# Kernel tuning notes

Hardware: AMD Instinct MI355X
Metric: run time of the kernel (lower is better)

Reference implementation:

```python
import jax, jax.numpy as jnp
import numpy as np

EMBED_DIM = 512
NUM_HEADS = 8
WINDOW = 128
B, S = 4, 2048


def setup_inputs() -> dict:
    key = jax.random.key(0)
    k0, k1, k2, k3, k4 = jax.random.split(key, 5)
    scale = 1.0 / np.sqrt(EMBED_DIM)
    return {
        "embeddings": jax.random.normal(k0, (B, S, EMBED_DIM), dtype=jnp.float32),
        "in_proj_w": jax.random.normal(k1, (3 * EMBED_DIM, EMBED_DIM), dtype=jnp.float32) * scale,
        "in_proj_b": jax.random.normal(k2, (3 * EMBED_DIM,), dtype=jnp.float32) * 0.01,
        "out_w": jax.random.normal(k3, (EMBED_DIM, EMBED_DIM), dtype=jnp.float32) * scale,
        "out_b": jax.random.normal(k4, (EMBED_DIM,), dtype=jnp.float32) * 0.01,
    }


def reference(embeddings, in_proj_w, in_proj_b, out_w, out_b):
    b, s, e = embeddings.shape
    h = NUM_HEADS
    dh = e // h
    # combined QKV projection (matches torch nn.MultiheadAttention in_proj)
    qkv = embeddings @ in_proj_w.T + in_proj_b          # [b,s,3e]
    q, k, v = jnp.split(qkv, 3, axis=-1)
    q = q.reshape(b, s, h, dh)
    k = k.reshape(b, s, h, dh)
    v = v.reshape(b, s, h, dh)
    scores = jnp.einsum("bihd,bjhd->bhij", q, k) / jnp.sqrt(jnp.float32(dh))
    # banded window mask: position i attends to [i-W, i+W]
    idx = jnp.arange(s)
    band = jnp.abs(idx[:, None] - idx[None, :]) <= WINDOW   # [s,s] bool
    scores = jnp.where(band, scores, -jnp.inf)
    attn = jax.nn.softmax(scores, axis=-1)                   # [b,h,s,s]
    ctx = jnp.einsum("bhij,bjhd->bihd", attn, v).reshape(b, s, e)
    out = ctx @ out_w.T + out_b                              # [b,s,e]
    pooled = jnp.max(out, axis=1)                            # [b,e]
    weights = jnp.mean(attn, axis=1)                         # head-averaged [b,s,s]
    return pooled, weights
```

## Files before the change

kernel.cpp:

```cpp
#include <hip/hip_runtime.h>
#include <math.h>

#define BB   4
#define SS   2048
#define EE   512
#define HH   8
#define DH   64
#define WW   128
#define MM   (BB*SS)
#define NTILE (SS/32)
#define SWH  296
#define VTP  296
#define WST  49
#define BK   64

typedef _Float16 f16x8 __attribute__((ext_vector_type(8)));
typedef _Float16 f16x2 __attribute__((ext_vector_type(2)));
typedef float    f32x4 __attribute__((ext_vector_type(4)));

#define GLOAD16(gp, lp) __builtin_amdgcn_global_load_lds( \
    (const __attribute__((address_space(1))) void*)(gp),  \
    (__attribute__((address_space(3))) void*)(lp), 16, 0, 0)

__global__ __launch_bounds__(256) void convert3(
    const float* __restrict__ a, const float* __restrict__ bsrc,
    const float* __restrict__ c,
    _Float16* __restrict__ da, _Float16* __restrict__ db, _Float16* __restrict__ dc)
{
    const size_t na4 = (size_t)MM*EE/4;
    const size_t nb4 = (size_t)3*EE*EE/4;
    const size_t nc4 = (size_t)EE*EE/4;
    const size_t tot = na4 + nb4 + nc4;
    for (size_t i = (size_t)blockIdx.x*256 + threadIdx.x; i < tot;
         i += (size_t)gridDim.x*256) {
        const float* s; _Float16* d; size_t off;
        if (i < na4)            { s = a;    d = da; off = i; }
        else if (i < na4 + nb4) { s = bsrc; d = db; off = i - na4; }
        else                    { s = c;    d = dc; off = i - na4 - nb4; }
        float4 v = ((const float4*)s)[off];
        union { _Float16 h[4]; uint2 u; } o;
        o.h[0] = (_Float16)v.x; o.h[1] = (_Float16)v.y;
        o.h[2] = (_Float16)v.z; o.h[3] = (_Float16)v.w;
        ((uint2*)d)[off] = o.u;
    }
}

__global__ __launch_bounds__(256) void qkv_mfma(
    const _Float16* __restrict__ A, const _Float16* __restrict__ Wt,
    const float* __restrict__ bias,
    _Float16* __restrict__ qd, _Float16* __restrict__ kd, _Float16* __restrict__ vd)
{
    __shared__ _Float16 As[128*BK];
    __shared__ _Float16 Bs[128*BK];

    const int tid = threadIdx.x;
    const int wid = tid >> 6, lane = tid & 63;
    const int l15 = lane & 15, g = lane >> 4;
    const int wr = wid >> 1, wc = wid & 1;
    const int m0 = blockIdx.x * 128;
    const int n0 = blockIdx.y * 128;

    const int lrow = lane >> 3;
    const int swz  = (lane & 7) ^ lrow;
    const _Float16* Ab = A  + (size_t)(m0 + wid*32 + lrow)*512 + swz*8;
    const _Float16* Bb = Wt + (size_t)(n0 + wid*32 + lrow)*512 + swz*8;

    f32x4 acc[4][4] = {};
    for (int k0 = 0; k0 < 512; k0 += BK) {
        __syncthreads();
        #pragma unroll
        for (int t = 0; t < 4; ++t) {
            GLOAD16(Ab + (size_t)t*8*512 + k0, &As[(wid*32 + t*8)*BK]);
            GLOAD16(Bb + (size_t)t*8*512 + k0, &Bs[(wid*32 + t*8)*BK]);
        }
        __syncthreads();

        f16x8 af[2][4], bf[2][4];
        #pragma unroll
        for (int ks = 0; ks < 2; ++ks)
            #pragma unroll
            for (int f = 0; f < 4; ++f) {
                const int ch = ((ks*4 + g) ^ (l15 & 7)) * 8;
                af[ks][f] = *(const f16x8*)&As[(wr*64 + f*16 + l15)*BK + ch];
                bf[ks][f] = *(const f16x8*)&Bs[(wc*64 + f*16 + l15)*BK + ch];
            }
        #pragma unroll
        for (int ks = 0; ks < 2; ++ks)
            #pragma unroll
            for (int fi = 0; fi < 4; ++fi)
                #pragma unroll
                for (int fj = 0; fj < 4; ++fj)
                    acc[fi][fj] = __builtin_amdgcn_mfma_f32_16x16x32_f16(
                        af[ks][fi], bf[ks][fj], acc[fi][fj], 0, 0, 0);
    }

    const int which = n0 >> 9;
    _Float16* dst = (which == 0) ? qd : (which == 1) ? kd : vd;
    #pragma unroll
    for (int fj = 0; fj < 4; ++fj) {
        const int col = n0 + wc*64 + fj*16 + l15;
        const int h = (col >> 6) & 7;
        const float bc = bias[col];
        #pragma unroll
        for (int fi = 0; fi < 4; ++fi)
            #pragma unroll
            for (int rr = 0; rr < 4; ++rr) {
                int grow = m0 + wr*64 + fi*16 + g*4 + rr;
                int b = grow >> 11, s = grow & 2047;
                dst[(((size_t)(b*HH + h))*SS + s)*DH + (col & 63)] =
                    (_Float16)(acc[fi][fj][rr] + bc);
            }
    }
}

__global__ __launch_bounds__(256) void out_mfma(
    const _Float16* __restrict__ A, const _Float16* __restrict__ Wt,
    const float* __restrict__ bias, float* __restrict__ part)
{
    __shared__ _Float16 As[128*BK];
    __shared__ _Float16 Bs[128*BK];

    const int tid = threadIdx.x;
    const int wid = tid >> 6, lane = tid & 63;
    const int l15 = lane & 15, g = lane >> 4;
    const int wr = wid >> 1, wc = wid & 1;
    const int m0 = blockIdx.x * 128;
    const int n0 = blockIdx.y * 128;

    const int lrow = lane >> 3;
    const int swz  = (lane & 7) ^ lrow;
    const _Float16* Ab = A  + (size_t)(m0 + wid*32 + lrow)*512 + swz*8;
    const _Float16* Bb = Wt + (size_t)(n0 + wid*32 + lrow)*512 + swz*8;

    f32x4 acc[4][4] = {};
    for (int k0 = 0; k0 < 512; k0 += BK) {
        __syncthreads();
        #pragma unroll
        for (int t = 0; t < 4; ++t) {
            GLOAD16(Ab + (size_t)t*8*512 + k0, &As[(wid*32 + t*8)*BK]);
            GLOAD16(Bb + (size_t)t*8*512 + k0, &Bs[(wid*32 + t*8)*BK]);
        }
        __syncthreads();

        f16x8 af[2][4], bf[2][4];
        #pragma unroll
        for (int ks = 0; ks < 2; ++ks)
            #pragma unroll
            for (int f = 0; f < 4; ++f) {
                const int ch = ((ks*4 + g) ^ (l15 & 7)) * 8;
                af[ks][f] = *(const f16x8*)&As[(wr*64 + f*16 + l15)*BK + ch];
                bf[ks][f] = *(const f16x8*)&Bs[(wc*64 + f*16 + l15)*BK + ch];
            }
        #pragma unroll
        for (int ks = 0; ks < 2; ++ks)
            #pragma unroll
            for (int fi = 0; fi < 4; ++fi)
                #pragma unroll
                for (int fj = 0; fj < 4; ++fj)
                    acc[fi][fj] = __builtin_amdgcn_mfma_f32_16x16x32_f16(
                        af[ks][fi], bf[ks][fj], acc[fi][fj], 0, 0, 0);
    }

    __syncthreads();
    float* red = (float*)As;
    #pragma unroll
    for (int fj = 0; fj < 4; ++fj) {
        float cm = -1e30f;
        #pragma unroll
        for (int fi = 0; fi < 4; ++fi)
            #pragma unroll
            for (int rr = 0; rr < 4; ++rr)
                cm = fmaxf(cm, acc[fi][fj][rr]);
        cm = fmaxf(cm, __shfl_xor(cm, 16));
        cm = fmaxf(cm, __shfl_xor(cm, 32));
        if (g == 0) red[wr*128 + wc*64 + fj*16 + l15] = cm;
    }
    __syncthreads();
    if (tid < 128) {
        float m = fmaxf(red[tid], red[128 + tid]) + bias[n0 + tid];
        part[(size_t)blockIdx.x * EE + n0 + tid] = m;
    }
}

__global__ __launch_bounds__(512, 4) void attn_mfma(
    const _Float16* __restrict__ qd, const _Float16* __restrict__ kd,
    const _Float16* __restrict__ vd, _Float16* __restrict__ ctx,
    float2* __restrict__ stats)
{
    __shared__ _Float16 sc[32 * SWH];
    __shared__ _Float16 vt[64 * VTP];

    const int tid  = threadIdx.x;
    const int wid  = tid >> 6;
    const int lane = tid & 63;
    const int l15  = lane & 15;
    const int g    = lane >> 4;

    const int lin = blockIdx.x + (blockIdx.y << 6) + (blockIdx.z << 8);
    const int nid = (lin & 7) * 256 + (lin >> 3);
    const int ti = nid & 63;
    const int b  = (nid >> 6) & 3;
    const int h  = nid >> 8;

    const int i0 = ti * 32;
    const int jlo = (i0 - WW > 0) ? i0 - WW : 0;
    const int jhi = (i0 + 31 + WW < SS - 1) ? i0 + 31 + WW : SS - 1;
    const int nj = jhi - jlo + 1;
    const int NC = nj >> 4;

    const _Float16* qb = qd + ((size_t)(b*HH + h))*SS*DH;
    const _Float16* kb = kd + ((size_t)(b*HH + h))*SS*DH;
    const _Float16* vb = vd + ((size_t)(b*HH + h))*SS*DH;

    for (int idx = tid; idx < 288*8; idx += 512) {
        int row = idx >> 3, dg = idx & 7;
        int d0 = dg * 8;
        int j = jlo + row;
        f16x8 vv = {};
        if (j <= jhi) vv = *(const f16x8*)(vb + (size_t)j*DH + d0);
        int blk = row >> 3, off = row & 7;
        int xb = (blk < 32) ? (blk ^ dg) : blk;
        _Float16* col = &vt[(size_t)d0*VTP + xb*8 + off];
        #pragma unroll
        for (int e = 0; e < 8; ++e)
            col[e*VTP] = vv[e];
    }

    if (nj < 288) {
        int row = tid >> 4, pt = tid & 15;
        for (int jj = nj + pt; jj < 288; jj += 16)
            sc[row*SWH + jj] = (_Float16)(-60000.f);
    }

    {
        const int rh = wid & 1, cgrp = wid >> 1;
        const int qrow = i0 + rh*16 + l15;
        f16x8 aq0 = *(const f16x8*)(qb + (size_t)qrow*DH +      g*8);
        f16x8 aq1 = *(const f16x8*)(qb + (size_t)qrow*DH + 32 + g*8);
        #pragma unroll
        for (int t = 0; t < 5; ++t) {
            int c = cgrp + t*4;
            if (c < NC) {
                int jj = c*16 + l15;
                int j  = jlo + jj;
                f16x8 bk0 = *(const f16x8*)(kb + (size_t)j*DH +      g*8);
                f16x8 bk1 = *(const f16x8*)(kb + (size_t)j*DH + 32 + g*8);
                f32x4 s = {0.f, 0.f, 0.f, 0.f};
                s = __builtin_amdgcn_mfma_f32_16x16x32_f16(aq0, bk0, s, 0, 0, 0);
                s = __builtin_amdgcn_mfma_f32_16x16x32_f16(aq1, bk1, s, 0, 0, 0);
                #pragma unroll
                for (int r = 0; r < 4; ++r) {
                    int srow = rh*16 + g*4 + r;
                    int i = i0 + srow;
                    int dd = i - j; if (dd < 0) dd = -dd;
                    float val = (dd <= WW) ? s[r]*0.125f : -60000.f;
                    sc[srow*SWH + jj] = (_Float16)val;
                }
            }
        }
    }
    __syncthreads();

    {
        const int qi = tid >> 4, pt = tid & 15;
        _Float16* srow = &sc[qi*SWH];
        f16x8 v0 = *(const f16x8*)&srow[pt*16];
        f16x8 v1 = *(const f16x8*)&srow[pt*16 + 8];
        f16x2 v2 = *(const f16x2*)&srow[256 + pt*2];
        float x[18];
        #pragma unroll
        for (int e = 0; e < 8; ++e) { x[e] = (float)v0[e]; x[8+e] = (float)v1[e]; }
        x[16] = (float)v2[0]; x[17] = (float)v2[1];

        float mrow = x[0];
        #pragma unroll
        for (int e = 1; e < 18; ++e) mrow = fmaxf(mrow, x[e]);
        #pragma unroll
        for (int o = 1; o < 16; o <<= 1) mrow = fmaxf(mrow, __shfl_xor(mrow, o));

        float ssum = 0.f;
        #pragma unroll
        for (int e = 0; e < 18; ++e) { x[e] = __expf(x[e] - mrow); ssum += x[e]; }
        #pragma unroll
        for (int o = 1; o < 16; o <<= 1) ssum += __shfl_xor(ssum, o);
        const float inv = 1.0f / ssum;

        f16x8 p0, p1;
        f16x2 p2;
        #pragma unroll
        for (int e = 0; e < 8; ++e) {
            p0[e] = (_Float16)(x[e]   * inv);
            p1[e] = (_Float16)(x[8+e] * inv);
        }
        p2[0] = (_Float16)(x[16] * inv);
        p2[1] = (_Float16)(x[17] * inv);
        *(f16x8*)&srow[pt*16]      = p0;
        *(f16x8*)&srow[pt*16 + 8]  = p1;
        *(f16x2*)&srow[256 + pt*2] = p2;
        if (pt == 0)
            stats[((size_t)(b*HH + h))*SS + i0 + qi] = make_float2(mrow, inv);
    }
    __syncthreads();

    {
        const int rh = wid & 1, dt = wid >> 1;
        const int d = dt*16 + l15;
        const int dg = d >> 3;
        f32x4 acc = {0.f, 0.f, 0.f, 0.f};
        #pragma unroll
        for (int ks = 0; ks < 9; ++ks) {
            int blk = ks*4 + g;
            int xb = (blk < 32) ? (blk ^ dg) : blk;
            f16x8 ap = *(const f16x8*)&sc[(rh*16 + l15)*SWH + ks*32 + g*8];
            f16x8 bv = *(const f16x8*)&vt[(size_t)d*VTP + xb*8];
            acc = __builtin_amdgcn_mfma_f32_16x16x32_f16(ap, bv, acc, 0, 0, 0);
        }
        #pragma unroll
        for (int r = 0; r < 4; ++r) {
            int row = i0 + rh*16 + g*4 + r;
            ctx[((size_t)(b*SS + row))*EE + h*DH + dt*16 + l15] = (_Float16)acc[r];
        }
    }
}

__global__ __launch_bounds__(256) void weights_k(
    const _Float16* __restrict__ qd, const _Float16* __restrict__ kd,
    const float2* __restrict__ stats, float* __restrict__ wout)
{
    __shared__ float wacc[32 * WST];

    const int tid  = threadIdx.x;
    const int wid  = tid >> 6;
    const int lane = tid & 63;
    const int l15  = lane & 15;
    const int g    = lane >> 4;

    const int lin = blockIdx.x + (blockIdx.y << 6) + (blockIdx.z << 8);
    const int nid = (lin & 7) * 192 + (lin >> 3);
    const int ti = nid & 63;
    const int b  = (nid >> 6) & 3;
    const int z  = nid >> 8;

    const int i0 = ti * 32;
    const int jlo = (i0 - WW > 0) ? i0 - WW : 0;
    const int jhi = (i0 + 31 + WW < SS - 1) ? i0 + 31 + WW : SS - 1;
    const int nj = jhi - jlo + 1;
    const int NC = nj >> 4;

    {
        const int L = jlo;
        const int Z = SS - nj;
        const int zrow = tid >> 3;
        const int zpt  = tid & 7;
        float* wrow = wout + ((size_t)(b*SS + i0 + zrow))*SS;
        int vend = (z + 1) * 320; if (vend > Z) vend = Z;
        const float4 zf = make_float4(0.f, 0.f, 0.f, 0.f);
        for (int v4 = z*320 + zpt*4; v4 < vend; v4 += 32) {
            int col = (v4 < L) ? v4 : (jhi + 1 + (v4 - L));
            *(float4*)(wrow + col) = zf;
        }
    }

    const int rh = wid & 1, cg2 = wid >> 1;
    const int qrow = i0 + rh*16 + l15;

    float ws[2][4];
    #pragma unroll
    for (int t = 0; t < 2; ++t)
        #pragma unroll
        for (int r = 0; r < 4; ++r) ws[t][r] = 0.f;

    for (int h = 0; h < HH; ++h) {
        const _Float16* qb = qd + ((size_t)(b*HH + h))*SS*DH;
        const _Float16* kb = kd + ((size_t)(b*HH + h))*SS*DH;
        f16x8 aq0 = *(const f16x8*)(qb + (size_t)qrow*DH +      g*8);
        f16x8 aq1 = *(const f16x8*)(qb + (size_t)qrow*DH + 32 + g*8);
        float2 st[4];
        #pragma unroll
        for (int r = 0; r < 4; ++r)
            st[r] = stats[((size_t)(b*HH + h))*SS + i0 + rh*16 + g*4 + r];

        #pragma unroll
        for (int t = 0; t < 2; ++t) {
            int lt = cg2 + t*2;
            int c = z*3 + lt;
            if (lt < 3 && c < NC) {
                int jj = c*16 + l15;
                int j  = jlo + jj;
                f16x8 bk0 = *(const f16x8*)(kb + (size_t)j*DH +      g*8);
                f16x8 bk1 = *(const f16x8*)(kb + (size_t)j*DH + 32 + g*8);
                f32x4 s = {0.f, 0.f, 0.f, 0.f};
                s = __builtin_amdgcn_mfma_f32_16x16x32_f16(aq0, bk0, s, 0, 0, 0);
                s = __builtin_amdgcn_mfma_f32_16x16x32_f16(aq1, bk1, s, 0, 0, 0);
                #pragma unroll
                for (int r = 0; r < 4; ++r) {
                    int i = i0 + rh*16 + g*4 + r;
                    int dd = i - j; if (dd < 0) dd = -dd;
                    if (dd <= WW)
                        ws[t][r] += __expf(s[r]*0.125f - st[r].x) * st[r].y;
                }
            }
        }
    }

    #pragma unroll
    for (int t = 0; t < 2; ++t) {
        int lt = cg2 + t*2, c = z*3 + lt;
        if (lt < 3 && c < NC) {
            #pragma unroll
            for (int r = 0; r < 4; ++r)
                wacc[(rh*16 + g*4 + r)*WST + lt*16 + l15] = ws[t][r];
        }
    }
    __syncthreads();

    const int cbase = jlo + z*48;
    int lo = cbase, hi = cbase + 48;
    if (hi > SS) hi = SS;

    const int row = tid >> 3;
    const int pt  = tid & 7;
    const int i = i0 + row;
    const int blo = (i - WW > 0) ? i - WW : 0;
    const int bhi = (i + WW < SS - 1) ? i + WW : SS - 1;
    float* wrow = wout + ((size_t)(b*SS + i))*SS;
    for (int j4 = lo + pt*4; j4 < hi; j4 += 32) {
        float4 o;
        float* oo = (float*)&o;
        #pragma unroll
        for (int e = 0; e < 4; ++e) {
            int j = j4 + e;
            oo[e] = (j >= blo && j <= bhi)
                  ? wacc[row*WST + (j - cbase)] * 0.125f : 0.f;
        }
        *(float4*)(wrow + j4) = o;
    }
}

__global__ void pool_final(const float* __restrict__ part, float* __restrict__ pooled)
{
    int e = blockIdx.x * 256 + threadIdx.x;
    int b = blockIdx.y;
    float m = -1e30f;
    #pragma unroll
    for (int t = 0; t < 16; ++t)
        m = fmaxf(m, part[((size_t)(b*16 + t))*EE + e]);
    pooled[b*EE + e] = m;
}

extern "C" void kernel_launch(void* const* d_in, const int* in_sizes, int n_in,
                              void* d_out, int out_size, void* d_ws, size_t ws_size,
                              hipStream_t stream)
{
    const float* emb = (const float*)d_in[0];
    const float* ipw = (const float*)d_in[1];
    const float* ipb = (const float*)d_in[2];
    const float* ow  = (const float*)d_in[3];
    const float* ob  = (const float*)d_in[4];

    float* pooled = (float*)d_out;
    float* wout   = pooled + (size_t)BB*EE;

    const size_t headsz = (size_t)BB*HH*SS*DH;
    _Float16* q    = (_Float16*)d_ws;
    _Float16* k    = q + headsz;
    _Float16* v    = k + headsz;
    _Float16* ctx  = v + headsz;
    _Float16* A16  = ctx + (size_t)MM*EE;
    _Float16* W16  = A16 + (size_t)MM*EE;
    _Float16* OW16 = W16 + (size_t)3*EE*EE;
    float* part    = (float*)(OW16 + (size_t)EE*EE);
    float2* stats  = (float2*)(part + 64*EE);

    convert3<<<1280, 256, 0, stream>>>(emb, ipw, ow, A16, W16, OW16);
    qkv_mfma<<<dim3(64, 12), 256, 0, stream>>>(A16, W16, ipb, q, k, v);
    attn_mfma<<<dim3(NTILE, BB, HH), 512, 0, stream>>>(q, k, v, ctx, stats);
    weights_k<<<dim3(NTILE, BB, 6), 256, 0, stream>>>(q, k, stats, wout);
    out_mfma<<<dim3(64, 4), 256, 0, stream>>>(ctx, OW16, ob, part);
    pool_final<<<dim3(2, BB), 256, 0, stream>>>(part, pooled);
}
```

Measured before the change: 111.9 us.

## Write V transposed from QKV GEMM and read it directly in attention

The QKV projection epilogue now stores V in a head-major transposed [b,h,d,s] layout. The attention kernel then feeds MFMA B-fragments straight from global memory instead of staging and transposing V through shared memory. Dropping the 37 KB vt LDS buffer lets launch_bounds request 8 blocks per CU instead of 4, raising occupancy. In exchange, the V writes in the QKV epilogue become strided 8-byte stores, the attention PV step now does global loads (the tail can read past the window, so 256 elements of padding were added), and the register budget per thread tightens.

```diff
diff --git a/kernel.cpp b/kernel.cpp
--- a/kernel.cpp
+++ b/kernel.cpp
@@ -10,7 +10,6 @@
 #define MM   (BB*SS)
 #define NTILE (SS/32)
 #define SWH  296
-#define VTP  296
 #define WST  49
 #define BK   64
 
@@ -48,7 +47,7 @@
 __global__ __launch_bounds__(256) void qkv_mfma(
     const _Float16* __restrict__ A, const _Float16* __restrict__ Wt,
     const float* __restrict__ bias,
-    _Float16* __restrict__ qd, _Float16* __restrict__ kd, _Float16* __restrict__ vd)
+    _Float16* __restrict__ qd, _Float16* __restrict__ kd, _Float16* __restrict__ vtg)
 {
     __shared__ _Float16 As[128*BK];
     __shared__ _Float16 Bs[128*BK];
@@ -95,21 +94,41 @@
     }
 
     const int which = n0 >> 9;
-    _Float16* dst = (which == 0) ? qd : (which == 1) ? kd : vd;
-    #pragma unroll
-    for (int fj = 0; fj < 4; ++fj) {
-        const int col = n0 + wc*64 + fj*16 + l15;
-        const int h = (col >> 6) & 7;
-        const float bc = bias[col];
-        #pragma unroll
-        for (int fi = 0; fi < 4; ++fi)
-            #pragma unroll
-            for (int rr = 0; rr < 4; ++rr) {
-                int grow = m0 + wr*64 + fi*16 + g*4 + rr;
-                int b = grow >> 11, s = grow & 2047;
-                dst[(((size_t)(b*HH + h))*SS + s)*DH + (col & 63)] =
-                    (_Float16)(acc[fi][fj][rr] + bc);
+    if (which < 2) {
+        _Float16* dst = (which == 0) ? qd : kd;
+        #pragma unroll
+        for (int fj = 0; fj < 4; ++fj) {
+            const int col = n0 + wc*64 + fj*16 + l15;
+            const int h = (col >> 6) & 7;
+            const float bc = bias[col];
+            #pragma unroll
+            for (int fi = 0; fi < 4; ++fi)
+                #pragma unroll
+                for (int rr = 0; rr < 4; ++rr) {
+                    int grow = m0 + wr*64 + fi*16 + g*4 + rr;
+                    int b = grow >> 11, s = grow & 2047;
+                    dst[(((size_t)(b*HH + h))*SS + s)*DH + (col & 63)] =
+                        (_Float16)(acc[fi][fj][rr] + bc);
+                }
+        }
+    } else {
+        #pragma unroll
+        for (int fj = 0; fj < 4; ++fj) {
+            const int col = n0 + wc*64 + fj*16 + l15;
+            const int h = (col >> 6) & 7;
+            const int d = col & 63;
+            const float bc = bias[col];
+            #pragma unroll
+            for (int fi = 0; fi < 4; ++fi) {
+                int grow0 = m0 + wr*64 + fi*16 + g*4;
+                int b = grow0 >> 11, s0 = grow0 & 2047;
+                union { _Float16 h4[4]; uint2 u; } o;
+                #pragma unroll
+                for (int rr = 0; rr < 4; ++rr)
+                    o.h4[rr] = (_Float16)(acc[fi][fj][rr] + bc);
+                *(uint2*)(vtg + (((size_t)(b*HH + h))*DH + d)*SS + s0) = o.u;
             }
+        }
     }
 }
 
@@ -182,13 +201,12 @@
     }
 }
 
-__global__ __launch_bounds__(512, 4) void attn_mfma(
+__global__ __launch_bounds__(512, 8) void attn_mfma(
     const _Float16* __restrict__ qd, const _Float16* __restrict__ kd,
-    const _Float16* __restrict__ vd, _Float16* __restrict__ ctx,
+    const _Float16* __restrict__ vtg, _Float16* __restrict__ ctx,
     float2* __restrict__ stats)
 {
     __shared__ _Float16 sc[32 * SWH];
-    __shared__ _Float16 vt[64 * VTP];
 
     const int tid  = threadIdx.x;
     const int wid  = tid >> 6;
@@ -208,23 +226,9 @@
     const int nj = jhi - jlo + 1;
     const int NC = nj >> 4;
 
-    const _Float16* qb = qd + ((size_t)(b*HH + h))*SS*DH;
-    const _Float16* kb = kd + ((size_t)(b*HH + h))*SS*DH;
-    const _Float16* vb = vd + ((size_t)(b*HH + h))*SS*DH;
-
-    for (int idx = tid; idx < 288*8; idx += 512) {
-        int row = idx >> 3, dg = idx & 7;
-        int d0 = dg * 8;
-        int j = jlo + row;
-        f16x8 vv = {};
-        if (j <= jhi) vv = *(const f16x8*)(vb + (size_t)j*DH + d0);
-        int blk = row >> 3, off = row & 7;
-        int xb = (blk < 32) ? (blk ^ dg) : blk;
-        _Float16* col = &vt[(size_t)d0*VTP + xb*8 + off];
-        #pragma unroll
-        for (int e = 0; e < 8; ++e)
-            col[e*VTP] = vv[e];
-    }
+    const _Float16* qb = qd  + ((size_t)(b*HH + h))*SS*DH;
+    const _Float16* kb = kd  + ((size_t)(b*HH + h))*SS*DH;
+    const _Float16* vb = vtg + ((size_t)(b*HH + h))*DH*SS;
 
     if (nj < 288) {
         int row = tid >> 4, pt = tid & 15;
@@ -305,20 +309,18 @@
     {
         const int rh = wid & 1, dt = wid >> 1;
         const int d = dt*16 + l15;
-        const int dg = d >> 3;
+        const _Float16* vrow = vb + (size_t)d*SS + jlo;
         f32x4 acc = {0.f, 0.f, 0.f, 0.f};
         #pragma unroll
         for (int ks = 0; ks < 9; ++ks) {
-            int blk = ks*4 + g;
-            int xb = (blk < 32) ? (blk ^ dg) : blk;
             f16x8 ap = *(const f16x8*)&sc[(rh*16 + l15)*SWH + ks*32 + g*8];
-            f16x8 bv = *(const f16x8*)&vt[(size_t)d*VTP + xb*8];
+            f16x8 bv = *(const f16x8*)(vrow + ks*32 + g*8);
             acc = __builtin_amdgcn_mfma_f32_16x16x32_f16(ap, bv, acc, 0, 0, 0);
         }
         #pragma unroll
         for (int r = 0; r < 4; ++r) {
             int row = i0 + rh*16 + g*4 + r;
-            ctx[((size_t)(b*SS + row))*EE + h*DH + dt*16 + l15] = (_Float16)acc[r];
+            ctx[((size_t)(b*SS + row))*EE + h*DH + d] = (_Float16)acc[r];
         }
     }
 }
@@ -464,8 +466,8 @@
     const size_t headsz = (size_t)BB*HH*SS*DH;
     _Float16* q    = (_Float16*)d_ws;
     _Float16* k    = q + headsz;
-    _Float16* v    = k + headsz;
-    _Float16* ctx  = v + headsz;
+    _Float16* vtg  = k + headsz;
+    _Float16* ctx  = vtg + headsz + 256;
     _Float16* A16  = ctx + (size_t)MM*EE;
     _Float16* W16  = A16 + (size_t)MM*EE;
     _Float16* OW16 = W16 + (size_t)3*EE*EE;
@@ -473,8 +475,8 @@
     float2* stats  = (float2*)(part + 64*EE);
 
     convert3<<<1280, 256, 0, stream>>>(emb, ipw, ow, A16, W16, OW16);
-    qkv_mfma<<<dim3(64, 12), 256, 0, stream>>>(A16, W16, ipb, q, k, v);
-    attn_mfma<<<dim3(NTILE, BB, HH), 512, 0, stream>>>(q, k, v, ctx, stats);
+    qkv_mfma<<<dim3(64, 12), 256, 0, stream>>>(A16, W16, ipb, q, k, vtg);
+    attn_mfma<<<dim3(NTILE, BB, HH), 512, 0, stream>>>(q, k, vtg, ctx, stats);
     weights_k<<<dim3(NTILE, BB, 6), 256, 0, stream>>>(q, k, stats, wout);
     out_mfma<<<dim3(64, 4), 256, 0, stream>>>(ctx, OW16, ob, part);
     pool_final<<<dim3(2, BB), 256, 0, stream>>>(part, pooled);
```

After: 119.0 us. 6.4% more time.
